# Optimization experiments

Measured on AMD Instinct MI355X. Metric: run time of the kernel, lower is better.

## Reference

```python
import jax, jax.numpy as jnp
import numpy as np

EMBED_DIM = 1024
NUM_HEADS = 16
HEAD_DIM = EMBED_DIM // NUM_HEADS
L, B, S = 2048, 2, 2048


def setup_inputs() -> dict:
    key = jax.random.key(0)
    kq, kk, kv = jax.random.split(key, 3)
    q = jax.random.normal(kq, (L, B, EMBED_DIM), dtype=jnp.float32)
    k = jax.random.normal(kk, (S, B, EMBED_DIM), dtype=jnp.float32)
    v = jax.random.normal(kv, (S, B, EMBED_DIM), dtype=jnp.float32)
    return {"q": q, "k": k, "v": v}


def reference(q, k, v):
    Lq, Bq, D = q.shape
    Sq = k.shape[0]
    scaling = HEAD_DIM ** -0.5
    # (L, B, D) -> (B*H, L, head_dim), matching reshape + transpose in torch
    qh = (q * scaling).reshape(Lq, Bq * NUM_HEADS, HEAD_DIM).transpose(1, 0, 2)
    kh = k.reshape(Sq, Bq * NUM_HEADS, HEAD_DIM).transpose(1, 0, 2)
    vh = v.reshape(Sq, Bq * NUM_HEADS, HEAD_DIM).transpose(1, 0, 2)
    # qk: (B*H, L, S) -- the full attention matrix the module materializes
    qk = jnp.einsum('ild,isd->ils', qh, kh)
    attn = jax.nn.softmax(qk, axis=-1)
    # dropout_p = 0.0 -> identity
    out = jnp.einsum('ils,isd->ild', attn, vh)  # (B*H, L, head_dim)
    out = out.transpose(1, 0, 2).reshape(Lq, Bq, D)
    return out
```

## Files before the change

### kernel.cpp

```cpp
#include <hip/hip_runtime.h>
#include <hip/hip_bf16.h>
#include <math.h>

typedef __bf16 bf16x8 __attribute__((ext_vector_type(8)));
typedef __bf16 bf16x4 __attribute__((ext_vector_type(4)));
typedef float  f32x4  __attribute__((ext_vector_type(4)));

constexpr int EMBED = 1024;
constexpr int NH    = 16;
constexpr int HD    = 64;
constexpr int LL    = 2048;
constexpr int BB    = 2;
constexpr int SSEQ  = 2048;

constexpr int BQ = 128;
constexpr int BK = 64;
constexpr int NT = SSEQ / BK;

constexpr size_t KW_ELEMS = (size_t)BB * NH * SSEQ * HD;

__device__ __forceinline__ void gload16(const void* g, void* l) {
  __builtin_amdgcn_global_load_lds((const __attribute__((address_space(1))) unsigned int*)g,
                                   (__attribute__((address_space(3))) unsigned int*)l, 16, 0, 0);
}

__device__ __forceinline__ float exp2_fast(float x) {
  float r;
  asm("v_exp_f32 %0, %1" : "=v"(r) : "v"(x));
  return r;
}

__global__ __launch_bounds__(256) void prep_kv(const float* __restrict__ Kg,
                                               const float* __restrict__ Vg,
                                               __hip_bfloat16* __restrict__ kw,
                                               __hip_bfloat16* __restrict__ vtw) {
  __shared__ char tsh[64 * 128];
  const int bid = blockIdx.x;
  if (bid < 2048) {
    const int idx = bid * 256 + threadIdx.x;
    const int e8 = idx & 127;
    const int t2 = idx >> 7;
    const int b  = t2 & 1;
    const int s  = t2 >> 1;
    const int h  = e8 >> 3;
    const int d8 = e8 & 7;
    const float* src = Kg + ((size_t)s * BB + b) * EMBED + e8 * 8;
    float4 a = *(const float4*)src;
    float4 c = *(const float4*)(src + 4);
    bf16x8 w;
    w[0] = (__bf16)a.x; w[1] = (__bf16)a.y; w[2] = (__bf16)a.z; w[3] = (__bf16)a.w;
    w[4] = (__bf16)c.x; w[5] = (__bf16)c.y; w[6] = (__bf16)c.z; w[7] = (__bf16)c.w;
    *(bf16x8*)(kw + (((size_t)(b * NH + h) * SSEQ + s) * HD + d8 * 8)) = w;
  } else {
    const int vb2 = bid - 2048;
    const int st  = vb2 & 31;
    const int bh  = vb2 >> 5;
    const int b   = bh >> 4;
    const int h   = bh & 15;
    const int t   = threadIdx.x;
    {
      const int r  = t >> 2;
      const int c0 = (t & 3) * 16;
      const float* src = Vg + ((size_t)(st * 64 + r) * BB + b) * EMBED + h * HD + c0;
      float4 x0 = *(const float4*)(src);
      float4 x1 = *(const float4*)(src + 4);
      float4 x2 = *(const float4*)(src + 8);
      float4 x3 = *(const float4*)(src + 12);
      bf16x8 w0, w1;
      w0[0] = (__bf16)x0.x; w0[1] = (__bf16)x0.y; w0[2] = (__bf16)x0.z; w0[3] = (__bf16)x0.w;
      w0[4] = (__bf16)x1.x; w0[5] = (__bf16)x1.y; w0[6] = (__bf16)x1.z; w0[7] = (__bf16)x1.w;
      w1[0] = (__bf16)x2.x; w1[1] = (__bf16)x2.y; w1[2] = (__bf16)x2.z; w1[3] = (__bf16)x2.w;
      w1[4] = (__bf16)x3.x; w1[5] = (__bf16)x3.y; w1[6] = (__bf16)x3.z; w1[7] = (__bf16)x3.w;
      const int colb = ((c0 + (r >> 3) * 16) & 63) * 2;
      char* rowp = tsh + r * 128;
      *(bf16x8*)(rowp + colb)      = w0;
      *(bf16x8*)(rowp + colb + 16) = w1;
    }
    __syncthreads();
    {
      const int d   = t >> 2;
      const int sc0 = (t & 3) * 16;
      bf16x8 o0, o1;
#pragma unroll
      for (int i = 0; i < 8; ++i) {
        const int s = sc0 + i;
        o0[i] = *(const __bf16*)(tsh + s * 128 + (((d + (s >> 3) * 16) & 63) * 2));
      }
#pragma unroll
      for (int i = 8; i < 16; ++i) {
        const int s = sc0 + i;
        o1[i - 8] = *(const __bf16*)(tsh + s * 128 + (((d + (s >> 3) * 16) & 63) * 2));
      }
      __hip_bfloat16* dst = vtw + ((size_t)(bh * HD + d)) * SSEQ + st * 64 + sc0;
      *(bf16x8*)(dst)     = o0;
      *(bf16x8*)(dst + 8) = o1;
    }
  }
}

__global__ __launch_bounds__(512) void sdpa_fwd(const float* __restrict__ Qg,
                                                const __hip_bfloat16* __restrict__ Kw,
                                                const __hip_bfloat16* __restrict__ VTw,
                                                float* __restrict__ Og) {
  __shared__ char sh[49152];
  char* kbuf = sh;
  char* vbuf = sh + 16384;
  char* psh  = sh + 32768;

  const int tid  = threadIdx.x;
  const int wv   = tid >> 6;
  const int lane = tid & 63;
  const int g    = lane >> 4;
  const int qc   = lane & 15;

  const int bid = blockIdx.x;
  const int xcd = bid & 7;
  const int rest = bid >> 3;
  const int qb  = rest & 15;
  const int bh  = ((rest >> 4) << 3) | xcd;
  const int bb  = bh >> 4;
  const int hh  = bh & 15;

  const size_t rstride = (size_t)BB * EMBED;
  const float* qb_ptr = Qg + (size_t)bb * EMBED + hh * HD;
  float*       ob     = Og + (size_t)bb * EMBED + hh * HD;
  const char*  kwb = (const char*)(Kw + (size_t)bh * SSEQ * HD);
  const char*  vtb = (const char*)(VTw + (size_t)bh * HD * SSEQ);

  const int qrow0 = qb * BQ + wv * 16;

  const int rW = wv * 8 + (lane >> 3);
  const int cW = (lane & 7) ^ (rW & 7);
  const char* kgS = kwb + rW * 128 + cW * 16;
  const char* vgS = vtb + (size_t)rW * 4096 + cW * 16;
  char* kdS = kbuf + wv * 1024;
  char* vdS = vbuf + wv * 1024;

#define STAGE(B, T)                                       \
  do {                                                    \
    gload16(kgS + (size_t)(T) * 8192, kdS + (B) * 8192);  \
    gload16(vgS + (size_t)(T) * 128,  vdS + (B) * 8192);  \
  } while (0)

  constexpr float QSC = 0.125f * 1.4426950408889634f;
  bf16x8 qf[2];
  {
    const float* qr = qb_ptr + (size_t)(qrow0 + qc) * rstride;
#pragma unroll
    for (int f = 0; f < 2; ++f) {
      const float* p = qr + f * 32 + g * 8;
      float4 a = *(const float4*)p;
      float4 c = *(const float4*)(p + 4);
      qf[f][0] = (__bf16)(a.x * QSC); qf[f][1] = (__bf16)(a.y * QSC);
      qf[f][2] = (__bf16)(a.z * QSC); qf[f][3] = (__bf16)(a.w * QSC);
      qf[f][4] = (__bf16)(c.x * QSC); qf[f][5] = (__bf16)(c.y * QSC);
      qf[f][6] = (__bf16)(c.z * QSC); qf[f][7] = (__bf16)(c.w * QSC);
    }
  }

  f32x4 acc[4];
#pragma unroll
  for (int nb = 0; nb < 4; ++nb) { acc[nb][0] = 0.f; acc[nb][1] = 0.f; acc[nb][2] = 0.f; acc[nb][3] = 0.f; }
  float m = -INFINITY;
  float l = 0.f;

  const int sw = (qc & 7) << 4;
  char* pw = psh + wv * 2048;

#define TILE(KOFF, VOFF)                                                      \
  do {                                                                        \
    const char* kb = kbuf + (KOFF);                                           \
    const char* vb = vbuf + (VOFF);                                           \
    f32x4 st[4];                                                              \
    __builtin_amdgcn_s_setprio(1);                                            \
    _Pragma("unroll")                                                         \
    for (int sb = 0; sb < 4; ++sb) {                                          \
      const int base = (sb * 16 + qc) * 128;                                  \
      bf16x8 k0 = *(const bf16x8*)(kb + base + ((g * 16)      ^ sw));         \
      bf16x8 k1 = *(const bf16x8*)(kb + base + ((64 + g * 16) ^ sw));         \
      f32x4 a; a[0] = 0.f; a[1] = 0.f; a[2] = 0.f; a[3] = 0.f;                \
      a = __builtin_amdgcn_mfma_f32_16x16x32_bf16(k0, qf[0], a, 0, 0, 0);     \
      a = __builtin_amdgcn_mfma_f32_16x16x32_bf16(k1, qf[1], a, 0, 0, 0);     \
      st[sb] = a;                                                             \
    }                                                                         \
    __builtin_amdgcn_s_setprio(0);                                            \
    float mx = fmaxf(fmaxf(fmaxf(st[0][0], st[0][1]), st[0][2]),              \
                     fmaxf(fmaxf(st[0][3], st[1][0]), st[1][1]));             \
    mx = fmaxf(mx, fmaxf(fmaxf(st[1][2], st[1][3]), st[2][0]));               \
    mx = fmaxf(mx, fmaxf(fmaxf(st[2][1], st[2][2]), st[2][3]));               \
    mx = fmaxf(mx, fmaxf(fmaxf(st[3][0], st[3][1]),                           \
                         fmaxf(st[3][2], st[3][3])));                         \
    mx = fmaxf(mx, __shfl_xor(mx, 16));                                       \
    mx = fmaxf(mx, __shfl_xor(mx, 32));                                       \
    if (!__all(mx - m <= 8.0f)) {                                             \
      const float mnew  = fmaxf(m, mx);                                       \
      const float alpha = exp2_fast(m - mnew);                                \
      m = mnew;                                                               \
      l *= alpha;                                                             \
      float ar[4];                                                            \
      _Pragma("unroll")                                                       \
      for (int r2 = 0; r2 < 4; ++r2) ar[r2] = __shfl(alpha, g * 4 + r2);      \
      _Pragma("unroll")                                                       \
      for (int nb = 0; nb < 4; ++nb)                                          \
        _Pragma("unroll")                                                     \
        for (int r2 = 0; r2 < 4; ++r2) acc[nb][r2] *= ar[r2];                 \
    }                                                                         \
    float rs = 0.f;                                                           \
    _Pragma("unroll")                                                         \
    for (int sb = 0; sb < 4; ++sb)                                            \
      _Pragma("unroll")                                                       \
      for (int r2 = 0; r2 < 4; ++r2) {                                        \
        float p = exp2_fast(st[sb][r2] - m);                                  \
        st[sb][r2] = p;                                                       \
        rs += p;                                                              \
      }                                                                       \
    rs += __shfl_xor(rs, 16);                                                 \
    rs += __shfl_xor(rs, 32);                                                 \
    l += rs;                                                                  \
    _Pragma("unroll")                                                         \
    for (int sb = 0; sb < 4; ++sb) {                                          \
      bf16x4 p4;                                                              \
      p4[0] = (__bf16)st[sb][0]; p4[1] = (__bf16)st[sb][1];                   \
      p4[2] = (__bf16)st[sb][2]; p4[3] = (__bf16)st[sb][3];                   \
      *(bf16x4*)(pw + qc * 128 + ((sb * 32 + g * 8) ^ sw)) = p4;              \
    }                                                                         \
    asm volatile("s_waitcnt lgkmcnt(0)" ::: "memory");                        \
    {                                                                         \
      bf16x8 pa0 = *(const bf16x8*)(pw + qc * 128 + ((g * 16)      ^ sw));    \
      bf16x8 pa1 = *(const bf16x8*)(pw + qc * 128 + ((64 + g * 16) ^ sw));    \
      __builtin_amdgcn_s_setprio(1);                                          \
      _Pragma("unroll")                                                       \
      for (int nb = 0; nb < 4; ++nb) {                                        \
        const int vbase = (nb * 16 + qc) * 128;                               \
        bf16x8 v0f = *(const bf16x8*)(vb + vbase + ((g * 16)      ^ sw));     \
        bf16x8 v1f = *(const bf16x8*)(vb + vbase + ((64 + g * 16) ^ sw));     \
        acc[nb] = __builtin_amdgcn_mfma_f32_16x16x32_bf16(pa0, v0f, acc[nb], 0, 0, 0); \
        acc[nb] = __builtin_amdgcn_mfma_f32_16x16x32_bf16(pa1, v1f, acc[nb], 0, 0, 0); \
      }                                                                       \
      __builtin_amdgcn_s_setprio(0);                                          \
    }                                                                         \
  } while (0)

  STAGE(0, 0);
  __syncthreads();

  for (int t = 0; t < NT; t += 2) {
    if (t + 1 < NT) STAGE(1, t + 1);
    TILE(0, 0);
    __syncthreads();
    if (t + 2 < NT) STAGE(0, t + 2);
    TILE(8192, 8192);
    __syncthreads();
  }
#undef STAGE
#undef TILE

  float linv[4];
#pragma unroll
  for (int r2 = 0; r2 < 4; ++r2) {
    float lr = __shfl(l, g * 4 + r2);
    linv[r2] = 1.0f / lr;
  }
#pragma unroll
  for (int nb = 0; nb < 4; ++nb)
#pragma unroll
    for (int r2 = 0; r2 < 4; ++r2) {
      const int row = qrow0 + g * 4 + r2;
      ob[(size_t)row * rstride + nb * 16 + qc] = acc[nb][r2] * linv[r2];
    }
}

extern "C" void kernel_launch(void* const* d_in, const int* in_sizes, int n_in,
                              void* d_out, int out_size, void* d_ws, size_t ws_size,
                              hipStream_t stream) {
  const float* q = (const float*)d_in[0];
  const float* k = (const float*)d_in[1];
  const float* v = (const float*)d_in[2];
  float* o = (float*)d_out;
  __hip_bfloat16* kw  = (__hip_bfloat16*)d_ws;
  __hip_bfloat16* vtw = kw + KW_ELEMS;

  prep_kv<<<dim3(3072), dim3(256), 0, stream>>>(k, v, kw, vtw);
  sdpa_fwd<<<dim3(512), dim3(512), 0, stream>>>(q, kw, vtw, o);
}
```

Baseline: 141.0 us.

## Process two 16-row query subtiles per wave with 4-wave blocks

Halves the block to 4 waves and gives each wave 32 query rows as two 16-row subtiles. The subtiles share the K and V fragments read from LDS, so LDS read traffic per MFMA drops, and each thread now issues twice as many global-to-LDS copies. The cost is roughly double the accumulator and score registers per wave and fewer waves per block to hide latency, which may lower occupancy.

```diff
diff --git a/kernel.cpp b/kernel.cpp
--- a/kernel.cpp
+++ b/kernel.cpp
@@ -98,7 +98,7 @@
   }
 }
 
-__global__ __launch_bounds__(512) void sdpa_fwd(const float* __restrict__ Qg,
+__global__ __launch_bounds__(256) void sdpa_fwd(const float* __restrict__ Qg,
                                                 const __hip_bfloat16* __restrict__ Kw,
                                                 const __hip_bfloat16* __restrict__ VTw,
                                                 float* __restrict__ Og) {
@@ -127,51 +127,106 @@
   const char*  kwb = (const char*)(Kw + (size_t)bh * SSEQ * HD);
   const char*  vtb = (const char*)(VTw + (size_t)bh * HD * SSEQ);
 
-  const int qrow0 = qb * BQ + wv * 16;
-
-  const int rW = wv * 8 + (lane >> 3);
-  const int cW = (lane & 7) ^ (rW & 7);
-  const char* kgS = kwb + rW * 128 + cW * 16;
-  const char* vgS = vtb + (size_t)rW * 4096 + cW * 16;
-  char* kdS = kbuf + wv * 1024;
-  char* vdS = vbuf + wv * 1024;
-
-#define STAGE(B, T)                                       \
-  do {                                                    \
-    gload16(kgS + (size_t)(T) * 8192, kdS + (B) * 8192);  \
-    gload16(vgS + (size_t)(T) * 128,  vdS + (B) * 8192);  \
+  const int qrow0 = qb * BQ + wv * 32;
+
+  const int rW0 = wv * 16 + (lane >> 3);
+  const int cW  = (lane & 7) ^ (rW0 & 7);
+  const char* kg0 = kwb + rW0 * 128 + cW * 16;
+  const char* vg0 = vtb + (size_t)rW0 * 4096 + cW * 16;
+  char* kdS = kbuf + wv * 2048;
+  char* vdS = vbuf + wv * 2048;
+
+#define STAGE(B, T)                                                 \
+  do {                                                              \
+    gload16(kg0 + (size_t)(T) * 8192,        kdS + (B) * 8192);     \
+    gload16(kg0 + (size_t)(T) * 8192 + 1024, kdS + (B) * 8192 + 1024); \
+    gload16(vg0 + (size_t)(T) * 128,             vdS + (B) * 8192);     \
+    gload16(vg0 + (size_t)(T) * 128 + 8 * 4096,  vdS + (B) * 8192 + 1024); \
   } while (0)
 
   constexpr float QSC = 0.125f * 1.4426950408889634f;
-  bf16x8 qf[2];
+  bf16x8 qfA[2], qfB[2];
   {
-    const float* qr = qb_ptr + (size_t)(qrow0 + qc) * rstride;
-#pragma unroll
-    for (int f = 0; f < 2; ++f) {
-      const float* p = qr + f * 32 + g * 8;
-      float4 a = *(const float4*)p;
-      float4 c = *(const float4*)(p + 4);
-      qf[f][0] = (__bf16)(a.x * QSC); qf[f][1] = (__bf16)(a.y * QSC);
-      qf[f][2] = (__bf16)(a.z * QSC); qf[f][3] = (__bf16)(a.w * QSC);
-      qf[f][4] = (__bf16)(c.x * QSC); qf[f][5] = (__bf16)(c.y * QSC);
-      qf[f][6] = (__bf16)(c.z * QSC); qf[f][7] = (__bf16)(c.w * QSC);
+#pragma unroll
+    for (int h2 = 0; h2 < 2; ++h2) {
+      const float* qr = qb_ptr + (size_t)(qrow0 + h2 * 16 + qc) * rstride;
+#pragma unroll
+      for (int f = 0; f < 2; ++f) {
+        const float* p = qr + f * 32 + g * 8;
+        float4 a = *(const float4*)p;
+        float4 c = *(const float4*)(p + 4);
+        bf16x8 w;
+        w[0] = (__bf16)(a.x * QSC); w[1] = (__bf16)(a.y * QSC);
+        w[2] = (__bf16)(a.z * QSC); w[3] = (__bf16)(a.w * QSC);
+        w[4] = (__bf16)(c.x * QSC); w[5] = (__bf16)(c.y * QSC);
+        w[6] = (__bf16)(c.z * QSC); w[7] = (__bf16)(c.w * QSC);
+        if (h2 == 0) qfA[f] = w; else qfB[f] = w;
+      }
     }
   }
 
-  f32x4 acc[4];
-#pragma unroll
-  for (int nb = 0; nb < 4; ++nb) { acc[nb][0] = 0.f; acc[nb][1] = 0.f; acc[nb][2] = 0.f; acc[nb][3] = 0.f; }
-  float m = -INFINITY;
-  float l = 0.f;
+  f32x4 accA[4], accB[4];
+#pragma unroll
+  for (int nb = 0; nb < 4; ++nb) {
+    accA[nb][0] = 0.f; accA[nb][1] = 0.f; accA[nb][2] = 0.f; accA[nb][3] = 0.f;
+    accB[nb][0] = 0.f; accB[nb][1] = 0.f; accB[nb][2] = 0.f; accB[nb][3] = 0.f;
+  }
+  float mA = -INFINITY, lA = 0.f;
+  float mB = -INFINITY, lB = 0.f;
 
   const int sw = (qc & 7) << 4;
-  char* pw = psh + wv * 2048;
-
-#define TILE(KOFF, VOFF)                                                      \
+  char* pwA = psh + wv * 4096;
+  char* pwB = pwA + 2048;
+
+#define SOFTMAX_PACK(ST, M, LSUM, ACC, PW)                                    \
   do {                                                                        \
-    const char* kb = kbuf + (KOFF);                                           \
-    const char* vb = vbuf + (VOFF);                                           \
-    f32x4 st[4];                                                              \
+    float mx = fmaxf(fmaxf(fmaxf(ST[0][0], ST[0][1]), ST[0][2]),              \
+                     fmaxf(fmaxf(ST[0][3], ST[1][0]), ST[1][1]));             \
+    mx = fmaxf(mx, fmaxf(fmaxf(ST[1][2], ST[1][3]), ST[2][0]));               \
+    mx = fmaxf(mx, fmaxf(fmaxf(ST[2][1], ST[2][2]), ST[2][3]));               \
+    mx = fmaxf(mx, fmaxf(fmaxf(ST[3][0], ST[3][1]),                           \
+                         fmaxf(ST[3][2], ST[3][3])));                         \
+    mx = fmaxf(mx, __shfl_xor(mx, 16));                                       \
+    mx = fmaxf(mx, __shfl_xor(mx, 32));                                       \
+    if (!__all(mx - M <= 8.0f)) {                                             \
+      const float mnew  = fmaxf(M, mx);                                       \
+      const float alpha = exp2_fast(M - mnew);                                \
+      M = mnew;                                                               \
+      LSUM *= alpha;                                                          \
+      float ar[4];                                                            \
+      _Pragma("unroll")                                                       \
+      for (int r2 = 0; r2 < 4; ++r2) ar[r2] = __shfl(alpha, g * 4 + r2);      \
+      _Pragma("unroll")                                                       \
+      for (int nb = 0; nb < 4; ++nb)                                          \
+        _Pragma("unroll")                                                     \
+        for (int r2 = 0; r2 < 4; ++r2) ACC[nb][r2] *= ar[r2];                 \
+    }                                                                         \
+    float rs = 0.f;                                                           \
+    _Pragma("unroll")                                                         \
+    for (int sb = 0; sb < 4; ++sb)                                            \
+      _Pragma("unroll")                                                       \
+      for (int r2 = 0; r2 < 4; ++r2) {                                        \
+        float p = exp2_fast(ST[sb][r2] - M);                                  \
+        ST[sb][r2] = p;                                                       \
+        rs += p;                                                              \
+      }                                                                       \
+    rs += __shfl_xor(rs, 16);                                                 \
+    rs += __shfl_xor(rs, 32);                                                 \
+    LSUM += rs;                                                               \
+    _Pragma("unroll")                                                         \
+    for (int sb = 0; sb < 4; ++sb) {                                          \
+      bf16x4 p4;                                                              \
+      p4[0] = (__bf16)ST[sb][0]; p4[1] = (__bf16)ST[sb][1];                   \
+      p4[2] = (__bf16)ST[sb][2]; p4[3] = (__bf16)ST[sb][3];                   \
+      *(bf16x4*)((PW) + qc * 128 + ((sb * 32 + g * 8) ^ sw)) = p4;            \
+    }                                                                         \
+  } while (0)
+
+#define TILE(OFF)                                                             \
+  do {                                                                        \
+    const char* kb = kbuf + (OFF);                                            \
+    const char* vb = vbuf + (OFF);                                            \
+    f32x4 stA[4], stB[4];                                                     \
     __builtin_amdgcn_s_setprio(1);                                            \
     _Pragma("unroll")                                                         \
     for (int sb = 0; sb < 4; ++sb) {                                          \
@@ -179,63 +234,33 @@
       bf16x8 k0 = *(const bf16x8*)(kb + base + ((g * 16)      ^ sw));         \
       bf16x8 k1 = *(const bf16x8*)(kb + base + ((64 + g * 16) ^ sw));         \
       f32x4 a; a[0] = 0.f; a[1] = 0.f; a[2] = 0.f; a[3] = 0.f;                \
-      a = __builtin_amdgcn_mfma_f32_16x16x32_bf16(k0, qf[0], a, 0, 0, 0);     \
-      a = __builtin_amdgcn_mfma_f32_16x16x32_bf16(k1, qf[1], a, 0, 0, 0);     \
-      st[sb] = a;                                                             \
+      f32x4 b; b[0] = 0.f; b[1] = 0.f; b[2] = 0.f; b[3] = 0.f;                \
+      a = __builtin_amdgcn_mfma_f32_16x16x32_bf16(k0, qfA[0], a, 0, 0, 0);    \
+      b = __builtin_amdgcn_mfma_f32_16x16x32_bf16(k0, qfB[0], b, 0, 0, 0);    \
+      a = __builtin_amdgcn_mfma_f32_16x16x32_bf16(k1, qfA[1], a, 0, 0, 0);    \
+      b = __builtin_amdgcn_mfma_f32_16x16x32_bf16(k1, qfB[1], b, 0, 0, 0);    \
+      stA[sb] = a;                                                            \
+      stB[sb] = b;                                                            \
     }                                                                         \
     __builtin_amdgcn_s_setprio(0);                                            \
-    float mx = fmaxf(fmaxf(fmaxf(st[0][0], st[0][1]), st[0][2]),              \
-                     fmaxf(fmaxf(st[0][3], st[1][0]), st[1][1]));             \
-    mx = fmaxf(mx, fmaxf(fmaxf(st[1][2], st[1][3]), st[2][0]));               \
-    mx = fmaxf(mx, fmaxf(fmaxf(st[2][1], st[2][2]), st[2][3]));               \
-    mx = fmaxf(mx, fmaxf(fmaxf(st[3][0], st[3][1]),                           \
-                         fmaxf(st[3][2], st[3][3])));                         \
-    mx = fmaxf(mx, __shfl_xor(mx, 16));                                       \
-    mx = fmaxf(mx, __shfl_xor(mx, 32));                                       \
-    if (!__all(mx - m <= 8.0f)) {                                             \
-      const float mnew  = fmaxf(m, mx);                                       \
-      const float alpha = exp2_fast(m - mnew);                                \
-      m = mnew;                                                               \
-      l *= alpha;                                                             \
-      float ar[4];                                                            \
-      _Pragma("unroll")                                                       \
-      for (int r2 = 0; r2 < 4; ++r2) ar[r2] = __shfl(alpha, g * 4 + r2);      \
-      _Pragma("unroll")                                                       \
-      for (int nb = 0; nb < 4; ++nb)                                          \
-        _Pragma("unroll")                                                     \
-        for (int r2 = 0; r2 < 4; ++r2) acc[nb][r2] *= ar[r2];                 \
-    }                                                                         \
-    float rs = 0.f;                                                           \
-    _Pragma("unroll")                                                         \
-    for (int sb = 0; sb < 4; ++sb)                                            \
-      _Pragma("unroll")                                                       \
-      for (int r2 = 0; r2 < 4; ++r2) {                                        \
-        float p = exp2_fast(st[sb][r2] - m);                                  \
-        st[sb][r2] = p;                                                       \
-        rs += p;                                                              \
-      }                                                                       \
-    rs += __shfl_xor(rs, 16);                                                 \
-    rs += __shfl_xor(rs, 32);                                                 \
-    l += rs;                                                                  \
-    _Pragma("unroll")                                                         \
-    for (int sb = 0; sb < 4; ++sb) {                                          \
-      bf16x4 p4;                                                              \
-      p4[0] = (__bf16)st[sb][0]; p4[1] = (__bf16)st[sb][1];                   \
-      p4[2] = (__bf16)st[sb][2]; p4[3] = (__bf16)st[sb][3];                   \
-      *(bf16x4*)(pw + qc * 128 + ((sb * 32 + g * 8) ^ sw)) = p4;              \
-    }                                                                         \
+    SOFTMAX_PACK(stA, mA, lA, accA, pwA);                                     \
+    SOFTMAX_PACK(stB, mB, lB, accB, pwB);                                     \
     asm volatile("s_waitcnt lgkmcnt(0)" ::: "memory");                        \
     {                                                                         \
-      bf16x8 pa0 = *(const bf16x8*)(pw + qc * 128 + ((g * 16)      ^ sw));    \
-      bf16x8 pa1 = *(const bf16x8*)(pw + qc * 128 + ((64 + g * 16) ^ sw));    \
+      bf16x8 paA0 = *(const bf16x8*)(pwA + qc * 128 + ((g * 16)      ^ sw));  \
+      bf16x8 paA1 = *(const bf16x8*)(pwA + qc * 128 + ((64 + g * 16) ^ sw));  \
+      bf16x8 paB0 = *(const bf16x8*)(pwB + qc * 128 + ((g * 16)      ^ sw));  \
+      bf16x8 paB1 = *(const bf16x8*)(pwB + qc * 128 + ((64 + g * 16) ^ sw));  \
       __builtin_amdgcn_s_setprio(1);                                          \
       _Pragma("unroll")                                                       \
       for (int nb = 0; nb < 4; ++nb) {                                        \
         const int vbase = (nb * 16 + qc) * 128;                               \
         bf16x8 v0f = *(const bf16x8*)(vb + vbase + ((g * 16)      ^ sw));     \
         bf16x8 v1f = *(const bf16x8*)(vb + vbase + ((64 + g * 16) ^ sw));     \
-        acc[nb] = __builtin_amdgcn_mfma_f32_16x16x32_bf16(pa0, v0f, acc[nb], 0, 0, 0); \
-        acc[nb] = __builtin_amdgcn_mfma_f32_16x16x32_bf16(pa1, v1f, acc[nb], 0, 0, 0); \
+        accA[nb] = __builtin_amdgcn_mfma_f32_16x16x32_bf16(paA0, v0f, accA[nb], 0, 0, 0); \
+        accB[nb] = __builtin_amdgcn_mfma_f32_16x16x32_bf16(paB0, v0f, accB[nb], 0, 0, 0); \
+        accA[nb] = __builtin_amdgcn_mfma_f32_16x16x32_bf16(paA1, v1f, accA[nb], 0, 0, 0); \
+        accB[nb] = __builtin_amdgcn_mfma_f32_16x16x32_bf16(paB1, v1f, accB[nb], 0, 0, 0); \
       }                                                                       \
       __builtin_amdgcn_s_setprio(0);                                          \
     }                                                                         \
@@ -246,28 +271,34 @@
 
   for (int t = 0; t < NT; t += 2) {
     if (t + 1 < NT) STAGE(1, t + 1);
-    TILE(0, 0);
+    TILE(0);
     __syncthreads();
     if (t + 2 < NT) STAGE(0, t + 2);
-    TILE(8192, 8192);
+    TILE(8192);
     __syncthreads();
   }
 #undef STAGE
 #undef TILE
-
-  float linv[4];
-#pragma unroll
-  for (int r2 = 0; r2 < 4; ++r2) {
-    float lr = __shfl(l, g * 4 + r2);
-    linv[r2] = 1.0f / lr;
-  }
-#pragma unroll
-  for (int nb = 0; nb < 4; ++nb)
+#undef SOFTMAX_PACK
+
+#pragma unroll
+  for (int h2 = 0; h2 < 2; ++h2) {
+    const float lv = (h2 == 0) ? lA : lB;
+    f32x4* acc = (h2 == 0) ? accA : accB;
+    float linv[4];
 #pragma unroll
     for (int r2 = 0; r2 < 4; ++r2) {
-      const int row = qrow0 + g * 4 + r2;
-      ob[(size_t)row * rstride + nb * 16 + qc] = acc[nb][r2] * linv[r2];
+      float lr = __shfl(lv, g * 4 + r2);
+      linv[r2] = 1.0f / lr;
     }
+#pragma unroll
+    for (int nb = 0; nb < 4; ++nb)
+#pragma unroll
+      for (int r2 = 0; r2 < 4; ++r2) {
+        const int row = qrow0 + h2 * 16 + g * 4 + r2;
+        ob[(size_t)row * rstride + nb * 16 + qc] = acc[nb][r2] * linv[r2];
+      }
+  }
 }
 
 extern "C" void kernel_launch(void* const* d_in, const int* in_sizes, int n_in,
@@ -281,5 +312,5 @@
   __hip_bfloat16* vtw = kw + KW_ELEMS;
 
   prep_kv<<<dim3(3072), dim3(256), 0, stream>>>(k, v, kw, vtw);
-  sdpa_fwd<<<dim3(512), dim3(512), 0, stream>>>(q, kw, vtw, o);
-}
+  sdpa_fwd<<<dim3(512), dim3(256), 0, stream>>>(q, kw, vtw, o);
+}
```

New measurement: 150.6 us. 6.8% more time.

## Load K tiles directly into registers instead of staging through LDS

Applied to the files above, without the earlier changes.

K fragments are now read from global memory straight into registers, one tile ahead and prefetched right after the QK MFMAs, so K no longer passes through shared memory. Only V stays double-buffered in LDS, which cuts shared memory from 48KB to 32KB, and launch bounds now request 4 blocks per SM to raise occupancy. The cost is more VGPRs for the prefetched K registers and uncoalesced-ish 16-byte global loads per lane that may stall the QK MFMAs if latency is not hidden.

```diff
diff --git a/kernel.cpp b/kernel.cpp
--- a/kernel.cpp
+++ b/kernel.cpp
@@ -98,14 +98,13 @@
   }
 }
 
-__global__ __launch_bounds__(512) void sdpa_fwd(const float* __restrict__ Qg,
-                                                const __hip_bfloat16* __restrict__ Kw,
-                                                const __hip_bfloat16* __restrict__ VTw,
-                                                float* __restrict__ Og) {
-  __shared__ char sh[49152];
-  char* kbuf = sh;
-  char* vbuf = sh + 16384;
-  char* psh  = sh + 32768;
+__global__ __launch_bounds__(512, 4) void sdpa_fwd(const float* __restrict__ Qg,
+                                                   const __hip_bfloat16* __restrict__ Kw,
+                                                   const __hip_bfloat16* __restrict__ VTw,
+                                                   float* __restrict__ Og) {
+  __shared__ char sh[32768];
+  char* vbuf = sh;
+  char* psh  = sh + 16384;
 
   const int tid  = threadIdx.x;
   const int wv   = tid >> 6;
@@ -131,15 +130,20 @@
 
   const int rW = wv * 8 + (lane >> 3);
   const int cW = (lane & 7) ^ (rW & 7);
-  const char* kgS = kwb + rW * 128 + cW * 16;
   const char* vgS = vtb + (size_t)rW * 4096 + cW * 16;
-  char* kdS = kbuf + wv * 1024;
   char* vdS = vbuf + wv * 1024;
 
-#define STAGE(B, T)                                       \
-  do {                                                    \
-    gload16(kgS + (size_t)(T) * 8192, kdS + (B) * 8192);  \
-    gload16(vgS + (size_t)(T) * 128,  vdS + (B) * 8192);  \
+#define STAGEV(B, T) gload16(vgS + (size_t)(T) * 128, vdS + (B) * 8192)
+
+  bf16x8 kf[8];
+#define LOADK(T)                                                              \
+  do {                                                                        \
+    _Pragma("unroll")                                                         \
+    for (int sb = 0; sb < 4; ++sb) {                                          \
+      const char* p_ = kwb + (size_t)((T) * 64 + sb * 16 + qc) * 128 + g * 16;\
+      kf[sb * 2 + 0] = *(const bf16x8*)(p_);                                  \
+      kf[sb * 2 + 1] = *(const bf16x8*)(p_ + 64);                             \
+    }                                                                         \
   } while (0)
 
   constexpr float QSC = 0.125f * 1.4426950408889634f;
@@ -167,23 +171,20 @@
   const int sw = (qc & 7) << 4;
   char* pw = psh + wv * 2048;
 
-#define TILE(KOFF, VOFF)                                                      \
+#define TILE(OFF, TNEXT, DOLOAD)                                              \
   do {                                                                        \
-    const char* kb = kbuf + (KOFF);                                           \
-    const char* vb = vbuf + (VOFF);                                           \
+    const char* vb = vbuf + (OFF);                                            \
     f32x4 st[4];                                                              \
     __builtin_amdgcn_s_setprio(1);                                            \
     _Pragma("unroll")                                                         \
     for (int sb = 0; sb < 4; ++sb) {                                          \
-      const int base = (sb * 16 + qc) * 128;                                  \
-      bf16x8 k0 = *(const bf16x8*)(kb + base + ((g * 16)      ^ sw));         \
-      bf16x8 k1 = *(const bf16x8*)(kb + base + ((64 + g * 16) ^ sw));         \
       f32x4 a; a[0] = 0.f; a[1] = 0.f; a[2] = 0.f; a[3] = 0.f;                \
-      a = __builtin_amdgcn_mfma_f32_16x16x32_bf16(k0, qf[0], a, 0, 0, 0);     \
-      a = __builtin_amdgcn_mfma_f32_16x16x32_bf16(k1, qf[1], a, 0, 0, 0);     \
+      a = __builtin_amdgcn_mfma_f32_16x16x32_bf16(kf[sb * 2 + 0], qf[0], a, 0, 0, 0); \
+      a = __builtin_amdgcn_mfma_f32_16x16x32_bf16(kf[sb * 2 + 1], qf[1], a, 0, 0, 0); \
       st[sb] = a;                                                             \
     }                                                                         \
     __builtin_amdgcn_s_setprio(0);                                            \
+    if (DOLOAD) LOADK(TNEXT);   \
     float mx = fmaxf(fmaxf(fmaxf(st[0][0], st[0][1]), st[0][2]),              \
                      fmaxf(fmaxf(st[0][3], st[1][0]), st[1][1]));             \
     mx = fmaxf(mx, fmaxf(fmaxf(st[1][2], st[1][3]), st[2][0]));               \
@@ -241,18 +242,20 @@
     }                                                                         \
   } while (0)
 
-  STAGE(0, 0);
+  LOADK(0);
+  STAGEV(0, 0);
   __syncthreads();
 
   for (int t = 0; t < NT; t += 2) {
-    if (t + 1 < NT) STAGE(1, t + 1);
-    TILE(0, 0);
+    if (t + 1 < NT) STAGEV(1, t + 1);
+    TILE(0, t + 1, t + 1 < NT);
     __syncthreads();
-    if (t + 2 < NT) STAGE(0, t + 2);
-    TILE(8192, 8192);
+    if (t + 2 < NT) STAGEV(0, t + 2);
+    TILE(8192, t + 2, t + 2 < NT);
     __syncthreads();
   }
-#undef STAGE
+#undef STAGEV
+#undef LOADK
 #undef TILE
 
   float linv[4];
```

New measurement: 215.1 us. 52.5% more time.
